# Kernel tuning notes

Measured on AMD Instinct MI355X. Metric: run time of the kernel, lower is better.

The kernel has to match this reference:

```python
import jax, jax.numpy as jnp
import numpy as np

N = 100000      # nodes on each bipartite side
E = 1600000     # edges
D_IN = 128      # input feature dim
H, C = 2, 50    # heads, per-head out channels
B = 64          # graphs in batch
NEG_SLOPE = 0.2 # GATConv leaky_relu slope


def setup_inputs() -> dict:
    key = jax.random.key(0)
    ks = jax.random.split(key, 12)
    glorot = lambda k, shape: (jax.random.uniform(k, shape, jnp.float32, -1.0, 1.0)
                               * jnp.sqrt(6.0 / (shape[0] + shape[-1])))
    return {
        "x_s": jax.random.normal(ks[0], (N, D_IN), jnp.float32),
        "x_t": jax.random.normal(ks[1], (N, D_IN), jnp.float32),
        "edge_index": jax.random.randint(ks[2], (2, E), 0, N, jnp.int64),
        "distances": jax.random.uniform(ks[3], (E,), jnp.float32),
        "x_s_batch": jnp.sort(jax.random.randint(ks[4], (N,), 0, B, jnp.int64)),
        "x_t_batch": jnp.sort(jax.random.randint(ks[5], (N,), 0, B, jnp.int64)),
        "W_src": glorot(ks[6], (D_IN, H * C)),
        "W_dst": glorot(ks[7], (D_IN, H * C)),
        "att_src": glorot(ks[8], (H, C)),
        "att_dst": glorot(ks[9], (H, C)),
        "bias_conv": jnp.zeros((H * C,), jnp.float32),
        "fc_w": glorot(ks[10], (H * C, 1)),
        "fc_b": jnp.zeros((1,), jnp.float32),
    }


def reference(x_s, x_t, edge_index, distances, x_s_batch, x_t_batch,
              W_src, W_dst, att_src, att_dst, bias_conv, fc_w, fc_b):
    src, dst = edge_index[0], edge_index[1]
    # Bipartite GATConv (edge_attr ignored: built with edge_dim=None)
    hs = (x_s @ W_src).reshape(N, H, C)            # [N,H,C]
    ht = (x_t @ W_dst).reshape(N, H, C)
    a_src = jnp.einsum('nhc,hc->nh', hs, att_src)  # [N,H]
    a_dst = jnp.einsum('nhc,hc->nh', ht, att_dst)
    e = jax.nn.leaky_relu(a_src[src] + a_dst[dst], NEG_SLOPE)   # [E,H]
    # segment softmax over edges sharing a target node
    m = jax.ops.segment_max(e, dst, num_segments=N)             # [N,H]
    ex = jnp.exp(e - m[dst])
    denom = jax.ops.segment_sum(ex, dst, num_segments=N)
    alpha = ex / (denom[dst] + 1e-16)                           # [E,H]
    # scatter-aggregate weighted source messages
    msg = alpha[:, :, None] * hs[src]                           # [E,H,C]
    out = jax.ops.segment_sum(msg, dst, num_segments=N)         # [N,H,C]
    out = out.reshape(N, H * C) + bias_conv
    x = jax.nn.relu(out)
    # global mean pool (original uses x_s_batch)
    pooled = jax.ops.segment_sum(x, x_s_batch, num_segments=B)
    counts = jax.ops.segment_sum(jnp.ones((N,), x.dtype), x_s_batch, num_segments=B)
    pooled = pooled / jnp.maximum(counts, 1.0)[:, None]         # [B,H*C]
    y = pooled @ fc_w + fc_b                                    # [B,1]
    return y.squeeze(-1)
```

## Files before the change

kernel.cpp:

```cpp
#include <hip/hip_runtime.h>
#include <math.h>

#define D_IN 128
#define HC 100
#define PW 128
#define CAP 64
#define NEG 0.2f
#define BINSH 6
#define NBIN 1563
#define BCAP 1408
#define ACH 4096
#define YSLOT 32
#define SRCM 0x1FFFF

typedef __attribute__((ext_vector_type(8))) short short8;
typedef __attribute__((ext_vector_type(4))) float f32x4;
typedef __attribute__((ext_vector_type(2))) float f32x2;

__device__ __forceinline__ float lrelu(float x){ return x > 0.f ? x : NEG*x; }

__device__ __forceinline__ unsigned short f2bf(float f){
  union { float f; unsigned u; } v; v.f = f;
  unsigned r = v.u + 0x7fffu + ((v.u >> 16) & 1u);
  return (unsigned short)(r >> 16);
}
__device__ __forceinline__ float bflo(unsigned u){
  union { unsigned x; float f; } v; v.x = u << 16; return v.f;
}
__device__ __forceinline__ float bfhi(unsigned u){
  union { unsigned x; float f; } v; v.x = u & 0xffff0000u; return v.f;
}

__global__ __launch_bounds__(256) void k_init(const float* __restrict__ Wd,
    const float* __restrict__ attd, const float* __restrict__ Ws,
    const float* __restrict__ bias, const float* __restrict__ fcw,
    const float* __restrict__ fcb, const int* __restrict__ xsb,
    float* __restrict__ wv, float* __restrict__ bias_p, float* __restrict__ fcwp,
    unsigned short* __restrict__ Wp, float* __restrict__ invb,
    int* __restrict__ bincnt, float* __restrict__ ypart,
    float* __restrict__ y, int N, int B){
  __shared__ int lo[257];
  int t = threadIdx.x;
  if (blockIdx.x == 0){
    int h = t >> 7, k = t & 127;
    float s = 0.f;
    #pragma unroll
    for (int c = 0; c < 50; ++c) s += Wd[k*HC + h*50 + c] * attd[h*50 + c];
    wv[t] = s;
    if (t < 128){
      bool cv = (t < 50) || (t >= 56 && t < 106);
      int c = (t < 50) ? t : t - 6;
      bias_p[t] = cv ? bias[c] : 0.f;
      fcwp[t]   = cv ? fcw[c]  : 0.f;
    }
    if (t < B) y[t] = fcb[0];
    for (int i = t; i < NBIN; i += 256) bincnt[i] = 0;
    if (t <= B && t < 257){
      int key = t, l = 0, hi = N;
      while (l < hi){ int mid = (l+hi)>>1; if (xsb[mid] < key) l = mid+1; else hi = mid; }
      lo[t] = l;
    }
    __syncthreads();
    if (t < B){
      int c = lo[t+1] - lo[t];
      invb[t] = 1.f / (float)((c > 0) ? c : 1);
    }
  } else if (blockIdx.x == 1){
    for (int idx = t; idx < 1792; idx += 256){
      int ct = idx >> 8, kk = (idx >> 6) & 3, lane = idx & 63;
      int kb = kk*32 + (lane >> 4)*8;
      int c  = ct*16 + (lane & 15);
      #pragma unroll
      for (int j = 0; j < 8; ++j){
        float v = (c < HC) ? Ws[(size_t)(kb + j)*HC + c] : 0.f;
        Wp[idx*8 + j] = f2bf(v);
      }
    }
  } else {
    float4 z = make_float4(0.f,0.f,0.f,0.f);
    float4* yp4 = (float4*)ypart + (size_t)(blockIdx.x - 2)*8192;
    for (int i = t; i < 8192; i += 256) yp4[i] = z;
  }
}

__global__ __launch_bounds__(256) void k_fused(
    const float* __restrict__ x_s, const unsigned short* __restrict__ Wp,
    const float* __restrict__ atts, unsigned short* __restrict__ hsb,
    float* __restrict__ a_src,
    const float* __restrict__ x_t, const float* __restrict__ wv,
    float* __restrict__ a_dst,
    const int* __restrict__ ei, int* __restrict__ bincnt,
    int* __restrict__ ebuf,
    int N, int E, int Gb)
{
  __shared__ __align__(16) unsigned char smem[17408];
  int t = threadIdx.x;
  int bid = blockIdx.x;

  if (bid >= Gb){
    unsigned short* hls = (unsigned short*)smem;
    float* wsh = (float*)(smem + 16384);
    int lane = t & 63, w = t >> 6;
    int qr = lane & 15, qq = lane >> 4;
    int row0 = (bid - Gb)*64;

    wsh[t] = wv[t];
    for (int i = t; i < 4096; i += 256) ((unsigned*)hls)[i] = 0u;

    int arow = row0 + w*16 + qr;
    bool rv = arow < N;
    short8 afr[4];
    const float* xp  = x_s + (size_t)arow*D_IN + qq*8;
    const float* xtp = x_t + (size_t)arow*D_IN + qq*8;
    #pragma unroll
    for (int kk = 0; kk < 4; ++kk){
      float4 v0 = make_float4(0.f,0.f,0.f,0.f), v1 = v0;
      if (rv){ v0 = *(const float4*)(xp + kk*32); v1 = *(const float4*)(xp + kk*32 + 4); }
      short8 a;
      a[0]=(short)f2bf(v0.x); a[1]=(short)f2bf(v0.y); a[2]=(short)f2bf(v0.z); a[3]=(short)f2bf(v0.w);
      a[4]=(short)f2bf(v1.x); a[5]=(short)f2bf(v1.y); a[6]=(short)f2bf(v1.z); a[7]=(short)f2bf(v1.w);
      afr[kk] = a;
    }
    float4 u[8];
    #pragma unroll
    for (int kk = 0; kk < 4; ++kk){
      u[2*kk]   = rv ? *(const float4*)(xtp + kk*32)     : make_float4(0.f,0.f,0.f,0.f);
      u[2*kk+1] = rv ? *(const float4*)(xtp + kk*32 + 4) : make_float4(0.f,0.f,0.f,0.f);
    }

    __syncthreads();

    float pd0 = 0.f, pd1 = 0.f;
    #pragma unroll
    for (int kk = 0; kk < 4; ++kk){
      float4 u0 = u[2*kk], u1 = u[2*kk+1];
      int kb = qq*8 + kk*32;
      pd0 += u0.x*wsh[kb+0] + u0.y*wsh[kb+1] + u0.z*wsh[kb+2] + u0.w*wsh[kb+3]
           + u1.x*wsh[kb+4] + u1.y*wsh[kb+5] + u1.z*wsh[kb+6] + u1.w*wsh[kb+7];
      pd1 += u0.x*wsh[128+kb+0] + u0.y*wsh[128+kb+1] + u0.z*wsh[128+kb+2] + u0.w*wsh[128+kb+3]
           + u1.x*wsh[128+kb+4] + u1.y*wsh[128+kb+5] + u1.z*wsh[128+kb+6] + u1.w*wsh[128+kb+7];
    }
    pd0 += __shfl_xor(pd0, 16, 64); pd0 += __shfl_xor(pd0, 32, 64);
    pd1 += __shfl_xor(pd1, 16, 64); pd1 += __shfl_xor(pd1, 32, 64);
    if (qq == 0 && rv){ a_dst[arow*2] = pd0; a_dst[arow*2+1] = pd1; }

    f32x4 acc[7];
    #pragma unroll
    for (int ct = 0; ct < 7; ++ct) acc[ct] = (f32x4){0.f,0.f,0.f,0.f};
    #pragma unroll
    for (int kk = 0; kk < 4; ++kk){
      #pragma unroll
      for (int ct = 0; ct < 7; ++ct){
        short8 b = *(const short8*)&Wp[(size_t)((ct*4+kk)*64 + lane)*8];
        acc[ct] = __builtin_amdgcn_mfma_f32_16x16x32_bf16(afr[kk], b, acc[ct], 0, 0, 0);
      }
    }

    float p0[4] = {0,0,0,0}, p1[4] = {0,0,0,0};
    #pragma unroll
    for (int ct = 0; ct < 7; ++ct){
      int c = ct*16 + qr;
      if (c < HC){
        float av = atts[c];
        #pragma unroll
        for (int r = 0; r < 4; ++r){
          float v = acc[ct][r];
          if (c < 50) p0[r] += v*av; else p1[r] += v*av;
        }
      }
    }
    #pragma unroll
    for (int d = 1; d < 16; d <<= 1){
      #pragma unroll
      for (int r = 0; r < 4; ++r){
        p0[r] += __shfl_xor(p0[r], d, 64);
        p1[r] += __shfl_xor(p1[r], d, 64);
      }
    }
    if (qr == 0){
      #pragma unroll
      for (int r = 0; r < 4; ++r){
        int row = row0 + w*16 + qq*4 + r;
        if (row < N){ a_src[row*2] = p0[r]; a_src[row*2+1] = p1[r]; }
      }
    }

    #pragma unroll
    for (int ct = 0; ct < 7; ++ct){
      int c = ct*16 + qr;
      if (c < HC){
        int p = (c < 50) ? c : c + 6;
        #pragma unroll
        for (int r = 0; r < 4; ++r)
          hls[(w*16 + qq*4 + r)*PW + p] = f2bf(acc[ct][r]);
      }
    }
    __syncthreads();
    unsigned* hg = (unsigned*)(hsb + (size_t)row0*PW);
    for (int i = t; i < 4096; i += 256) hg[i] = ((unsigned*)hls)[i];

  } else {
    int* cnt   = (int*)smem;
    int* gbase = (int*)smem + NBIN;
    int e0 = bid * ACH;
    for (int i = t; i < NBIN; i += 256) cnt[i] = 0;
    __syncthreads();

    int src[16], dst[16], rank[16];
    #pragma unroll
    for (int j = 0; j < 4; ++j){
      int e = e0 + t*16 + j*4;
      bool in = (e + 4 <= E);
      int4 s4 = in ? *(const int4*)&ei[e]     : make_int4(0,0,0,0);
      int4 d4 = in ? *(const int4*)&ei[E + e] : make_int4(-1,-1,-1,-1);
      src[j*4+0]=s4.x; src[j*4+1]=s4.y; src[j*4+2]=s4.z; src[j*4+3]=s4.w;
      dst[j*4+0]=d4.x; dst[j*4+1]=d4.y; dst[j*4+2]=d4.z; dst[j*4+3]=d4.w;
    }
    #pragma unroll
    for (int j = 0; j < 16; ++j)
      rank[j] = (dst[j] >= 0) ? atomicAdd(&cnt[dst[j] >> BINSH], 1) : -1;
    __syncthreads();
    for (int i = t; i < NBIN; i += 256)
      gbase[i] = (cnt[i] > 0) ? atomicAdd(&bincnt[i], cnt[i]) : 0;
    __syncthreads();
    #pragma unroll
    for (int j = 0; j < 16; ++j){
      if (rank[j] >= 0){
        int b = dst[j] >> BINSH;
        int gp = gbase[b] + rank[j];
        if (gp < BCAP) ebuf[(size_t)b*BCAP + gp] = src[j] | ((dst[j] & 63) << 17);
      }
    }
  }
}

__global__ __launch_bounds__(128) void k_agg(const int* __restrict__ bincnt,
    const int* __restrict__ ebuf, const float* __restrict__ a_src,
    const float* __restrict__ a_dst, const unsigned short* __restrict__ hsb,
    const float* __restrict__ bias_p, const float* __restrict__ fcwp,
    const int* __restrict__ xsb, float* __restrict__ ypart, int N)
{
  __shared__ int lsrc[32*CAP];
  __shared__ int lcnt[32];
  int t = threadIdx.x, b = blockIdx.x;
  int bin = b >> 1, half = b & 1;
  if (t < 32) lcnt[t] = 0;
  __syncthreads();
  int nE = bincnt[bin]; if (nE > BCAP) nE = BCAP;
  const int* eb = ebuf + (size_t)bin*BCAP;
  for (int i = t; i < nE; i += 128){
    int e = eb[i];
    int ld = (e >> 17) & 63;
    if ((ld >> 5) == half){
      int p = atomicAdd(&lcnt[ld & 31], 1);
      if (p < CAP) lsrc[(ld & 31)*CAP + p] = e & SRCM;
    }
  }
  __syncthreads();

  int lane = t & 63, w = t >> 6;
  int k = lane & 15, g = lane >> 4;
  bool actv = (k < 14);
  bool hsel = (k >= 7);

#define PREF(vv, e) { int s_ = __shfl(sreg, (e), 64); \
    vv = (actv && (e) < deg) ? *(const uint4*)&hsb[(size_t)s_*PW + k*8] \
                             : make_uint4(0u,0u,0u,0u); }

#define CONS(vv, e) { float a0_ = __shfl(al0, (e), 64); float a1_ = __shfl(al1, (e), 64); \
    float a_ = hsel ? a1_ : a0_; f32x2 av_ = {a_, a_}; \
    f32x2 h0_ = {bflo(vv.x), bfhi(vv.x)}; acc0 += av_*h0_; \
    f32x2 h1_ = {bflo(vv.y), bfhi(vv.y)}; acc1 += av_*h1_; \
    f32x2 h2_ = {bflo(vv.z), bfhi(vv.z)}; acc2 += av_*h2_; \
    f32x2 h3_ = {bflo(vv.w), bfhi(vv.w)}; acc3 += av_*h3_; }

  for (int it = 0; it < 16; ++it){
    int nl = w*16 + it;
    int n  = bin*64 + half*32 + nl;
    if (n >= N) break;
    int deg = lcnt[nl]; if (deg > CAP) deg = CAP;
    float2 ad = *(const float2*)&a_dst[n*2];
    int sreg = (lane < deg) ? lsrc[nl*CAP + lane] : 0;

    uint4 v0, v1, v2, v3;
    PREF(v0, g) PREF(v1, 4+g) PREF(v2, 8+g) PREF(v3, 12+g)

    float e0 = -INFINITY, e1 = -INFINITY;
    if (lane < deg){
      float2 as = *(const float2*)&a_src[sreg*2];
      e0 = lrelu(as.x + ad.x);
      e1 = lrelu(as.y + ad.y);
    }
    float m0 = e0, m1 = e1;
    if (deg > 32){ m0 = fmaxf(m0, __shfl_xor(m0,32,64)); m1 = fmaxf(m1, __shfl_xor(m1,32,64)); }
    if (deg > 16){ m0 = fmaxf(m0, __shfl_xor(m0,16,64)); m1 = fmaxf(m1, __shfl_xor(m1,16,64)); }
    #pragma unroll
    for (int d = 8; d >= 1; d >>= 1){
      m0 = fmaxf(m0, __shfl_xor(m0,d,64)); m1 = fmaxf(m1, __shfl_xor(m1,d,64));
    }
    float x0 = 0.f, x1 = 0.f;
    if (lane < deg){ x0 = __expf(e0 - m0); x1 = __expf(e1 - m1); }
    float d0 = x0, d1 = x1;
    if (deg > 32){ d0 += __shfl_xor(d0,32,64); d1 += __shfl_xor(d1,32,64); }
    if (deg > 16){ d0 += __shfl_xor(d0,16,64); d1 += __shfl_xor(d1,16,64); }
    #pragma unroll
    for (int d = 8; d >= 1; d >>= 1){ d0 += __shfl_xor(d0,d,64); d1 += __shfl_xor(d1,d,64); }
    float inv0 = __builtin_amdgcn_rcpf(d0 + 1e-16f);
    float inv1 = __builtin_amdgcn_rcpf(d1 + 1e-16f);
    float al0 = x0 * inv0, al1 = x1 * inv1;

    f32x2 acc0 = {0.f,0.f}, acc1 = {0.f,0.f}, acc2 = {0.f,0.f}, acc3 = {0.f,0.f};
    int base = 0;
    for (;;){
      CONS(v0, base+g);
      if (base + 4 >= deg) break;
      CONS(v1, base+4+g);
      if (base + 8 >= deg) break;
      CONS(v2, base+8+g);
      if (base + 12 >= deg) break;
      CONS(v3, base+12+g);
      base += 16;
      if (base >= deg) break;
      PREF(v0, base+g) PREF(v1, base+4+g) PREF(v2, base+8+g) PREF(v3, base+12+g)
    }

    float acc[8] = {acc0.x, acc0.y, acc1.x, acc1.y, acc2.x, acc2.y, acc3.x, acc3.y};
    #pragma unroll
    for (int j = 0; j < 8; ++j){
      acc[j] += __shfl_xor(acc[j], 16, 64);
      acc[j] += __shfl_xor(acc[j], 32, 64);
    }

    float s = 0.f;
    if (g == 0 && actv){
      float4 b0 = *(const float4*)&bias_p[k*8];
      float4 b1 = *(const float4*)&bias_p[k*8 + 4];
      float4 f0 = *(const float4*)&fcwp[k*8];
      float4 f1 = *(const float4*)&fcwp[k*8 + 4];
      s  = fmaxf(acc[0]+b0.x, 0.f)*f0.x + fmaxf(acc[1]+b0.y, 0.f)*f0.y
         + fmaxf(acc[2]+b0.z, 0.f)*f0.z + fmaxf(acc[3]+b0.w, 0.f)*f0.w
         + fmaxf(acc[4]+b1.x, 0.f)*f1.x + fmaxf(acc[5]+b1.y, 0.f)*f1.y
         + fmaxf(acc[6]+b1.z, 0.f)*f1.z + fmaxf(acc[7]+b1.w, 0.f)*f1.w;
    }
    #pragma unroll
    for (int d = 1; d <= 8; d <<= 1) s += __shfl_xor(s, d, 64);
    if (lane == 0){
      int bb = xsb[n];
      atomicAdd(&ypart[(size_t)((bb*YSLOT + (b & (YSLOT-1))) << 5)], s);
    }
  }
#undef PREF
#undef CONS
}

__global__ __launch_bounds__(64) void k_red(const float* __restrict__ ypart,
    const float* __restrict__ invb, float* __restrict__ y)
{
  int b = blockIdx.x, t = threadIdx.x;
  float v = (t < YSLOT) ? ypart[(size_t)((b*YSLOT + t) << 5)] : 0.f;
  #pragma unroll
  for (int d = 16; d >= 1; d >>= 1) v += __shfl_xor(v, d, 64);
  if (t == 0) y[b] += v * invb[b];
}

extern "C" void kernel_launch(void* const* d_in, const int* in_sizes, int n_in,
                              void* d_out, int out_size, void* d_ws, size_t ws_size,
                              hipStream_t stream)
{
  const float* x_s  = (const float*)d_in[0];
  const float* x_t  = (const float*)d_in[1];
  const int*   ei   = (const int*)d_in[2];
  const int*   xsb  = (const int*)d_in[4];
  const float* Ws   = (const float*)d_in[6];
  const float* Wd   = (const float*)d_in[7];
  const float* atts = (const float*)d_in[8];
  const float* attd = (const float*)d_in[9];
  const float* bias = (const float*)d_in[10];
  const float* fcw  = (const float*)d_in[11];
  const float* fcb  = (const float*)d_in[12];
  float* y = (float*)d_out;

  const int N = in_sizes[4];
  const int E = in_sizes[3];
  const int B = out_size;

  char* p = (char*)d_ws;
  auto carve = [&](size_t bytes)->char*{
    char* r = p; p += (bytes + 255) & ~(size_t)255; return r;
  };
  float*          wv     = (float*)         carve(256*4);
  float*          a_src  = (float*)         carve((size_t)N*2*4);
  float*          a_dst  = (float*)         carve((size_t)N*2*4);
  unsigned short* hsb    = (unsigned short*)carve((size_t)(N+64)*PW*2);
  float*          bias_p = (float*)         carve(128*4);
  float*          fcwp   = (float*)         carve(128*4);
  unsigned short* Wp     = (unsigned short*)carve((size_t)1792*8*2);
  float*          invb   = (float*)         carve(256*4);
  int*            bincnt = (int*)           carve(2048*4);
  float*          ypart  = (float*)         carve((size_t)B*YSLOT*32*4);
  int*            ebuf   = (int*)           carve((size_t)NBIN*BCAP*4);

  const int Gg = (N + 63) / 64;
  const int Gb = (E + ACH - 1) / ACH;

  k_init  <<<4, 256, 0, stream>>>(Wd, attd, Ws, bias, fcw, fcb, xsb,
                                  wv, bias_p, fcwp, Wp, invb, bincnt, ypart, y, N, B);
  k_fused <<<Gb + Gg, 256, 0, stream>>>(x_s, Wp, atts, hsb, a_src,
                                        x_t, wv, a_dst,
                                        ei, bincnt, ebuf, N, E, Gb);
  k_agg   <<<NBIN*2, 128, 0, stream>>>(bincnt, ebuf, a_src, a_dst, hsb,
                                       bias_p, fcwp, xsb, ypart, N);
  k_red   <<<B, 64, 0, stream>>>(ypart, invb, y);
}
```

Baseline: 275.9 us.

## Drop softmax max pass and move a_dst projection into edge-binning blocks

The segment softmax in the aggregation kernel no longer computes a per-node max with shuffle reductions. It exponentiates the leaky-relu logits directly, clamped at 60 to avoid overflow, which removes one wave-wide reduction per node. This is exact only when logits stay well below the clamp, so it trades numerical robustness on large-magnitude inputs for fewer instructions. Separately, the x_t·w projection that produces a_dst moves from the MFMA GEMM blocks into the edge-binning blocks, which read x_t rows with a wave-wide shuffle reduction. This is meant to balance work between the two block types and shorten the GEMM path.

```diff
diff --git a/kernel.cpp b/kernel.cpp
--- a/kernel.cpp
+++ b/kernel.cpp
@@ -99,19 +99,16 @@
 
   if (bid >= Gb){
     unsigned short* hls = (unsigned short*)smem;
-    float* wsh = (float*)(smem + 16384);
     int lane = t & 63, w = t >> 6;
     int qr = lane & 15, qq = lane >> 4;
     int row0 = (bid - Gb)*64;
 
-    wsh[t] = wv[t];
     for (int i = t; i < 4096; i += 256) ((unsigned*)hls)[i] = 0u;
 
     int arow = row0 + w*16 + qr;
     bool rv = arow < N;
     short8 afr[4];
-    const float* xp  = x_s + (size_t)arow*D_IN + qq*8;
-    const float* xtp = x_t + (size_t)arow*D_IN + qq*8;
+    const float* xp = x_s + (size_t)arow*D_IN + qq*8;
     #pragma unroll
     for (int kk = 0; kk < 4; ++kk){
       float4 v0 = make_float4(0.f,0.f,0.f,0.f), v1 = v0;
@@ -121,28 +118,6 @@
       a[4]=(short)f2bf(v1.x); a[5]=(short)f2bf(v1.y); a[6]=(short)f2bf(v1.z); a[7]=(short)f2bf(v1.w);
       afr[kk] = a;
     }
-    float4 u[8];
-    #pragma unroll
-    for (int kk = 0; kk < 4; ++kk){
-      u[2*kk]   = rv ? *(const float4*)(xtp + kk*32)     : make_float4(0.f,0.f,0.f,0.f);
-      u[2*kk+1] = rv ? *(const float4*)(xtp + kk*32 + 4) : make_float4(0.f,0.f,0.f,0.f);
-    }
-
-    __syncthreads();
-
-    float pd0 = 0.f, pd1 = 0.f;
-    #pragma unroll
-    for (int kk = 0; kk < 4; ++kk){
-      float4 u0 = u[2*kk], u1 = u[2*kk+1];
-      int kb = qq*8 + kk*32;
-      pd0 += u0.x*wsh[kb+0] + u0.y*wsh[kb+1] + u0.z*wsh[kb+2] + u0.w*wsh[kb+3]
-           + u1.x*wsh[kb+4] + u1.y*wsh[kb+5] + u1.z*wsh[kb+6] + u1.w*wsh[kb+7];
-      pd1 += u0.x*wsh[128+kb+0] + u0.y*wsh[128+kb+1] + u0.z*wsh[128+kb+2] + u0.w*wsh[128+kb+3]
-           + u1.x*wsh[128+kb+4] + u1.y*wsh[128+kb+5] + u1.z*wsh[128+kb+6] + u1.w*wsh[128+kb+7];
-    }
-    pd0 += __shfl_xor(pd0, 16, 64); pd0 += __shfl_xor(pd0, 32, 64);
-    pd1 += __shfl_xor(pd1, 16, 64); pd1 += __shfl_xor(pd1, 32, 64);
-    if (qq == 0 && rv){ a_dst[arow*2] = pd0; a_dst[arow*2+1] = pd1; }
 
     f32x4 acc[7];
     #pragma unroll
@@ -185,6 +160,7 @@
       }
     }
 
+    __syncthreads();
     #pragma unroll
     for (int ct = 0; ct < 7; ++ct){
       int c = ct*16 + qr;
@@ -202,7 +178,9 @@
   } else {
     int* cnt   = (int*)smem;
     int* gbase = (int*)smem + NBIN;
+    float* wsh = (float*)(smem + 12544);
     int e0 = bid * ACH;
+    wsh[t] = wv[t];
     for (int i = t; i < NBIN; i += 256) cnt[i] = 0;
     __syncthreads();
 
@@ -230,6 +208,24 @@
         int gp = gbase[b] + rank[j];
         if (gp < BCAP) ebuf[(size_t)b*BCAP + gp] = src[j] | ((dst[j] & 63) << 17);
       }
+    }
+
+    int lane = t & 63, w = t >> 6;
+    int rbase = bid*256 + w*64;
+    float w0a = wsh[lane*2],     w0b = wsh[lane*2+1];
+    float w1a = wsh[128+lane*2], w1b = wsh[128+lane*2+1];
+    #pragma unroll 2
+    for (int rr = 0; rr < 64; ++rr){
+      int row = rbase + rr;
+      if (row >= N) break;
+      float2 x2 = *(const float2*)&x_t[(size_t)row*D_IN + lane*2];
+      float p0 = x2.x*w0a + x2.y*w0b;
+      float p1 = x2.x*w1a + x2.y*w1b;
+      #pragma unroll
+      for (int d = 32; d >= 1; d >>= 1){
+        p0 += __shfl_xor(p0, d, 64); p1 += __shfl_xor(p1, d, 64);
+      }
+      if (lane == 0){ a_dst[row*2] = p0; a_dst[row*2+1] = p1; }
     }
   }
 }
@@ -285,21 +281,12 @@
     uint4 v0, v1, v2, v3;
     PREF(v0, g) PREF(v1, 4+g) PREF(v2, 8+g) PREF(v3, 12+g)
 
-    float e0 = -INFINITY, e1 = -INFINITY;
+    float x0 = 0.f, x1 = 0.f;
     if (lane < deg){
       float2 as = *(const float2*)&a_src[sreg*2];
-      e0 = lrelu(as.x + ad.x);
-      e1 = lrelu(as.y + ad.y);
-    }
-    float m0 = e0, m1 = e1;
-    if (deg > 32){ m0 = fmaxf(m0, __shfl_xor(m0,32,64)); m1 = fmaxf(m1, __shfl_xor(m1,32,64)); }
-    if (deg > 16){ m0 = fmaxf(m0, __shfl_xor(m0,16,64)); m1 = fmaxf(m1, __shfl_xor(m1,16,64)); }
-    #pragma unroll
-    for (int d = 8; d >= 1; d >>= 1){
-      m0 = fmaxf(m0, __shfl_xor(m0,d,64)); m1 = fmaxf(m1, __shfl_xor(m1,d,64));
-    }
-    float x0 = 0.f, x1 = 0.f;
-    if (lane < deg){ x0 = __expf(e0 - m0); x1 = __expf(e1 - m1); }
+      x0 = __expf(fminf(lrelu(as.x + ad.x), 60.f));
+      x1 = __expf(fminf(lrelu(as.y + ad.y), 60.f));
+    }
     float d0 = x0, d1 = x1;
     if (deg > 32){ d0 += __shfl_xor(d0,32,64); d1 += __shfl_xor(d1,32,64); }
     if (deg > 16){ d0 += __shfl_xor(d0,16,64); d1 += __shfl_xor(d1,16,64); }
```

Measured after the change: 290.3 us. +5.2%, slower.
